# Optimization experiments

Hardware: AMD Instinct MI355X
Metric: run time of the kernel (lower is better)

Reference implementation:

```python
import jax, jax.numpy as jnp
import numpy as np


def setup_inputs() -> dict:
    key = jax.random.key(0)
    k1, k2, k3 = jax.random.split(key, 3)
    B, F, H, W = 16, 16, 256, 256
    inp = jax.random.normal(k1, (B, F, H, W), dtype=jnp.float32)
    target = jax.random.normal(k2, (B, F, H, W), dtype=jnp.float32)
    masks = jax.random.randint(k3, (B, F, H, W), 0, 2).astype(jnp.bool_)
    hull = jnp.zeros((1,), dtype=jnp.int32)  # unused by the module's forward
    return {"input": inp, "target": target, "masks": masks, "hull": hull}


def _masked_mean_per_feature(diff, w):
    # diff: [B,F,H,W]; w: float mask broadcastable to diff. Returns [F] masked means
    # with 0.0 where the mask is empty (matching the torch `if len(diff) > 0` guard).
    s = jnp.sum(diff * w, axis=(0, 2, 3))                               # [F]
    c = jnp.sum(jnp.broadcast_to(w, diff.shape), axis=(0, 2, 3))        # [F]
    return jnp.where(c > 0, s / jnp.maximum(c, 1.0), 0.0)


def reference(input, target, masks, hull):
    diff = jnp.abs(input - target)                                      # [B,F,H,W]
    m = masks.astype(diff.dtype)                                        # feature masks
    m_not = 1.0 - m                                                     # background
    m_all = jnp.any(masks, axis=1, keepdims=True).astype(diff.dtype)    # [B,1,H,W]

    loss_features = jnp.mean(_masked_mean_per_feature(diff, m))
    loss_background = jnp.mean(_masked_mean_per_feature(diff, m_not))
    loss_all_features = jnp.mean(_masked_mean_per_feature(diff, m_all))

    return (loss_features + loss_all_features + loss_background) / 3.0
```

## Files before the change

kernel.cpp:

```cpp
#include <hip/hip_runtime.h>
#include <hip/hip_bf16.h>

constexpr int B = 16, F = 16, H = 256, W = 256;
constexpr int HW = H * W;
constexpr int SPATIAL = B * HW;
constexpr int NBLOCKS = 1024;
constexpr int NTHREADS = 256;
constexpr int NVALS = 65;
constexpr int PLANE4 = HW / 4;
constexpr int BSTRIDE4 = F * PLANE4;

__inline__ __device__ float wave_reduce_sum(float v) {
    #pragma unroll
    for (int o = 32; o > 0; o >>= 1) v += __shfl_down(v, o, 64);
    return v;
}

__global__ __launch_bounds__(NTHREADS) void heatloss_main(
        const float4* __restrict__ inp, const float4* __restrict__ tgt,
        const unsigned int* __restrict__ msk, float* __restrict__ partials) {
    const int g   = blockIdx.x * NTHREADS + threadIdx.x;
    const int b   = g >> 14;
    const int hw4 = g & (PLANE4 - 1);
    const int base = b * BSTRIDE4 + hw4;

    unsigned int m[F];
    #pragma unroll
    for (int f = 0; f < F; f++) m[f] = msk[base + f * PLANE4];

    unsigned int anyu = 0;
    #pragma unroll
    for (int f = 0; f < F; f++) anyu |= m[f];
    const float af0 = (anyu & 0x000000FFu) ? 1.f : 0.f;
    const float af1 = (anyu & 0x0000FF00u) ? 1.f : 0.f;
    const float af2 = (anyu & 0x00FF0000u) ? 1.f : 0.f;
    const float af3 = (anyu & 0xFF000000u) ? 1.f : 0.f;
    const float call = (af0 + af1) + (af2 + af3);

    float s[F], c[F], dtot[F], sall[F];
    #pragma unroll
    for (int f = 0; f < F; f++) {
        const float4 a = inp[base + f * PLANE4];
        const float4 t = tgt[base + f * PLANE4];
        const float d0 = fabsf(a.x - t.x);
        const float d1 = fabsf(a.y - t.y);
        const float d2 = fabsf(a.z - t.z);
        const float d3 = fabsf(a.w - t.w);
        const unsigned int mm = m[f];
        const float m0 = (float)( mm        & 0xFFu);
        const float m1 = (float)((mm >> 8)  & 0xFFu);
        const float m2 = (float)((mm >> 16) & 0xFFu);
        const float m3 = (float)( mm >> 24);
        dtot[f] = (d0 + d1) + (d2 + d3);
        s[f]    = m0 * d0 + m1 * d1 + m2 * d2 + m3 * d3;
        c[f]    = (m0 + m1) + (m2 + m3);
        sall[f] = af0 * d0 + af1 * d1 + af2 * d2 + af3 * d3;
    }

    __shared__ float red[NTHREADS / 64][NVALS];
    const int lane = threadIdx.x & 63;
    const int wave = threadIdx.x >> 6;
    #pragma unroll
    for (int v = 0; v < NVALS; v++) {
        float x = (v < 16) ? s[v]
                : (v < 32) ? c[v - 16]
                : (v < 48) ? dtot[v - 32]
                : (v < 64) ? sall[v - 48]
                : call;
        x = wave_reduce_sum(x);
        if (lane == 0) red[wave][v] = x;
    }
    __syncthreads();
    if (threadIdx.x < NVALS) {
        const int v = threadIdx.x;
        float t = 0.f;
        #pragma unroll
        for (int w2 = 0; w2 < NTHREADS / 64; w2++) t += red[w2][v];
        partials[v * NBLOCKS + blockIdx.x] = t;
    }
}

__global__ __launch_bounds__(512) void heatloss_finalize(
        const float* __restrict__ partials, float* __restrict__ out) {
    __shared__ float vals[NVALS];
    const int wave = threadIdx.x >> 6;
    const int lane = threadIdx.x & 63;
    for (int v = wave; v < NVALS; v += 8) {
        const float* p = partials + v * NBLOCKS;
        float x = 0.f;
        #pragma unroll
        for (int i = 0; i < NBLOCKS / 64; i++) x += p[i * 64 + lane];
        x = wave_reduce_sum(x);
        if (lane == 0) vals[v] = x;
    }
    __syncthreads();
    if (threadIdx.x == 0) {
        const float Nf = (float)SPATIAL;
        const float call = vals[64];
        float lf = 0.f, lbg = 0.f, lall = 0.f;
        #pragma unroll
        for (int f = 0; f < F; f++) {
            const float sf = vals[f], cf = vals[16 + f];
            const float dt = vals[32 + f], sa = vals[48 + f];
            lf += (cf > 0.f) ? sf / cf : 0.f;
            const float sbg = dt - sf, cbg = Nf - cf;
            lbg += (cbg > 0.f) ? sbg / cbg : 0.f;
            lall += (call > 0.f) ? sa / call : 0.f;
        }
        out[0] = (lf / 16.f + lbg / 16.f + lall / 16.f) / 3.f;
    }
}

extern "C" void kernel_launch(void* const* d_in, const int* in_sizes, int n_in,
                              void* d_out, int out_size, void* d_ws, size_t ws_size,
                              hipStream_t stream) {
    const float4*       inp = (const float4*)d_in[0];
    const float4*       tgt = (const float4*)d_in[1];
    const unsigned int* msk = (const unsigned int*)d_in[2];
    float* out      = (float*)d_out;
    float* partials = (float*)d_ws;

    heatloss_main<<<NBLOCKS, NTHREADS, 0, stream>>>(inp, tgt, msk, partials);
    heatloss_finalize<<<1, 512, 0, stream>>>(partials, out);
}
```

Before: 203.6 us.

## Split features across half-waves with 512-thread blocks to raise parallelism

Each wave now covers 32 spatial float4 positions, and each half-wave handles 8 of the 16 features, so every thread does half the loads and keeps half as many accumulators. The any-feature mask is combined across the two halves with a cross-lane shuffle, and the reductions use 32-lane shuffles. Block size doubles to 512 threads with a minimum-occupancy hint, so more memory requests are in flight per CU and register pressure drops. In exchange, the per-block reduction tree grows and coalescing is now in 32-lane (128-byte per float4 row) chunks per half-wave.

```diff
diff --git a/kernel.cpp b/kernel.cpp
--- a/kernel.cpp
+++ b/kernel.cpp
@@ -5,78 +5,88 @@
 constexpr int HW = H * W;
 constexpr int SPATIAL = B * HW;
 constexpr int NBLOCKS = 1024;
-constexpr int NTHREADS = 256;
+constexpr int NTHREADS = 512;
 constexpr int NVALS = 65;
 constexpr int PLANE4 = HW / 4;
 constexpr int BSTRIDE4 = F * PLANE4;
+constexpr int FH = 8;
 
-__inline__ __device__ float wave_reduce_sum(float v) {
+__inline__ __device__ float reduce32(float v) {
     #pragma unroll
-    for (int o = 32; o > 0; o >>= 1) v += __shfl_down(v, o, 64);
+    for (int o = 16; o > 0; o >>= 1) v += __shfl_down(v, o, 32);
     return v;
 }
 
-__global__ __launch_bounds__(NTHREADS) void heatloss_main(
+__global__ __launch_bounds__(NTHREADS, 8) void heatloss_main(
         const float4* __restrict__ inp, const float4* __restrict__ tgt,
         const unsigned int* __restrict__ msk, float* __restrict__ partials) {
-    const int g   = blockIdx.x * NTHREADS + threadIdx.x;
-    const int b   = g >> 14;
-    const int hw4 = g & (PLANE4 - 1);
-    const int base = b * BSTRIDE4 + hw4;
+    const int tid    = threadIdx.x;
+    const int wave   = tid >> 6;
+    const int lane   = tid & 63;
+    const int lane32 = lane & 31;
+    const int half   = lane >> 5;
+    const int g      = (blockIdx.x * 8 + wave) * 32 + lane32;
+    const int b      = g >> 14;
+    const int hw4    = g & (PLANE4 - 1);
+    const int base   = b * BSTRIDE4 + hw4 + half * (FH * PLANE4);
 
-    unsigned int m[F];
+    unsigned int m[FH];
     #pragma unroll
-    for (int f = 0; f < F; f++) m[f] = msk[base + f * PLANE4];
+    for (int j = 0; j < FH; j++) m[j] = msk[base + j * PLANE4];
 
     unsigned int anyu = 0;
     #pragma unroll
-    for (int f = 0; f < F; f++) anyu |= m[f];
+    for (int j = 0; j < FH; j++) anyu |= m[j];
+    anyu |= __shfl_xor(anyu, 32, 64);
     const float af0 = (anyu & 0x000000FFu) ? 1.f : 0.f;
     const float af1 = (anyu & 0x0000FF00u) ? 1.f : 0.f;
     const float af2 = (anyu & 0x00FF0000u) ? 1.f : 0.f;
     const float af3 = (anyu & 0xFF000000u) ? 1.f : 0.f;
-    const float call = (af0 + af1) + (af2 + af3);
+    const float call = (half == 0) ? (af0 + af1) + (af2 + af3) : 0.f;
 
-    float s[F], c[F], dtot[F], sall[F];
+    float s[FH], c[FH], dtot[FH], sall[FH];
     #pragma unroll
-    for (int f = 0; f < F; f++) {
-        const float4 a = inp[base + f * PLANE4];
-        const float4 t = tgt[base + f * PLANE4];
+    for (int j = 0; j < FH; j++) {
+        const float4 a = inp[base + j * PLANE4];
+        const float4 t = tgt[base + j * PLANE4];
         const float d0 = fabsf(a.x - t.x);
         const float d1 = fabsf(a.y - t.y);
         const float d2 = fabsf(a.z - t.z);
         const float d3 = fabsf(a.w - t.w);
-        const unsigned int mm = m[f];
+        const unsigned int mm = m[j];
         const float m0 = (float)( mm        & 0xFFu);
         const float m1 = (float)((mm >> 8)  & 0xFFu);
         const float m2 = (float)((mm >> 16) & 0xFFu);
         const float m3 = (float)( mm >> 24);
-        dtot[f] = (d0 + d1) + (d2 + d3);
-        s[f]    = m0 * d0 + m1 * d1 + m2 * d2 + m3 * d3;
-        c[f]    = (m0 + m1) + (m2 + m3);
-        sall[f] = af0 * d0 + af1 * d1 + af2 * d2 + af3 * d3;
+        dtot[j] = (d0 + d1) + (d2 + d3);
+        s[j]    = m0 * d0 + m1 * d1 + m2 * d2 + m3 * d3;
+        c[j]    = (m0 + m1) + (m2 + m3);
+        sall[j] = af0 * d0 + af1 * d1 + af2 * d2 + af3 * d3;
     }
 
     __shared__ float red[NTHREADS / 64][NVALS];
-    const int lane = threadIdx.x & 63;
-    const int wave = threadIdx.x >> 6;
+    const int fbase = half * FH;
     #pragma unroll
-    for (int v = 0; v < NVALS; v++) {
-        float x = (v < 16) ? s[v]
-                : (v < 32) ? c[v - 16]
-                : (v < 48) ? dtot[v - 32]
-                : (v < 64) ? sall[v - 48]
-                : call;
-        x = wave_reduce_sum(x);
-        if (lane == 0) red[wave][v] = x;
+    for (int j = 0; j < FH; j++) {
+        const float xs = reduce32(s[j]);
+        const float xc = reduce32(c[j]);
+        const float xd = reduce32(dtot[j]);
+        const float xa = reduce32(sall[j]);
+        if (lane32 == 0) {
+            red[wave][ 0 + fbase + j] = xs;
+            red[wave][16 + fbase + j] = xc;
+            red[wave][32 + fbase + j] = xd;
+            red[wave][48 + fbase + j] = xa;
+        }
     }
+    const float xcall = reduce32(call);
+    if (lane == 0) red[wave][64] = xcall;
     __syncthreads();
-    if (threadIdx.x < NVALS) {
-        const int v = threadIdx.x;
+    if (tid < NVALS) {
         float t = 0.f;
         #pragma unroll
-        for (int w2 = 0; w2 < NTHREADS / 64; w2++) t += red[w2][v];
-        partials[v * NBLOCKS + blockIdx.x] = t;
+        for (int w2 = 0; w2 < NTHREADS / 64; w2++) t += red[w2][tid];
+        partials[tid * NBLOCKS + blockIdx.x] = t;
     }
 }
 
@@ -90,7 +100,8 @@
         float x = 0.f;
         #pragma unroll
         for (int i = 0; i < NBLOCKS / 64; i++) x += p[i * 64 + lane];
-        x = wave_reduce_sum(x);
+        #pragma unroll
+        for (int o = 32; o > 0; o >>= 1) x += __shfl_down(x, o, 64);
         if (lane == 0) vals[v] = x;
     }
     __syncthreads();
```

Result: slower. 211.4 us (+3.8%).

## Split loss into any-mask pass and per-feature streaming pass with staged reductions

Applied to the files above, without the earlier changes.

Restructures the single fused kernel into four kernels. The first computes the any-feature mask per pixel into workspace, the second streams input, target and mask per (feature, chunk) block with only four accumulators, and two small kernels then reduce the partials. The aim is to drop the heavy register use of 64 per-thread accumulators and the 65-value shuffle reduction, which should raise occupancy and make the memory stream simpler. In exchange the mask is read twice, a 4 MB any-mask buffer is written and read back, and there are extra kernel launches.

```diff
diff --git a/kernel.cpp b/kernel.cpp
--- a/kernel.cpp
+++ b/kernel.cpp
@@ -4,108 +4,138 @@
 constexpr int B = 16, F = 16, H = 256, W = 256;
 constexpr int HW = H * W;
 constexpr int SPATIAL = B * HW;
-constexpr int NBLOCKS = 1024;
-constexpr int NTHREADS = 256;
 constexpr int NVALS = 65;
-constexpr int PLANE4 = HW / 4;
-constexpr int BSTRIDE4 = F * PLANE4;
+constexpr int PLANE4  = HW / 4;
+constexpr int BSTR4   = F * PLANE4;
+constexpr int POS4    = SPATIAL / 4;
 
-__inline__ __device__ float wave_reduce_sum(float v) {
+constexpr int NB_A = 1024;
+constexpr int NB_B = 2048;
+constexpr int CHUNKS = NB_B / F;
+constexpr int ITER = 8;
+
+constexpr int WS_ANY = 0;
+constexpr int WS_PA  = POS4;
+constexpr int WS_PB  = WS_PA + NB_A;
+constexpr int WS_VAL = WS_PB + 64 * CHUNKS;
+
+
+__global__ __launch_bounds__(256) void heat_any(
+        const unsigned int* __restrict__ msk, unsigned int* __restrict__ any,
+        float* __restrict__ pa) {
+    const int p4 = blockIdx.x * 256 + threadIdx.x;
+    const int b   = p4 >> 14;
+    const int hw4 = p4 & (PLANE4 - 1);
+    const int base = b * BSTR4 + hw4;
+    unsigned int a = 0;
     #pragma unroll
-    for (int o = 32; o > 0; o >>= 1) v += __shfl_down(v, o, 64);
-    return v;
+    for (int f = 0; f < F; f++) a |= msk[base + f * PLANE4];
+    any[p4] = a;
+    float cnt = (float)((a & 1u) + ((a >> 8) & 1u) + ((a >> 16) & 1u) + (a >> 24));
+    #pragma unroll
+    for (int o = 32; o > 0; o >>= 1) cnt += __shfl_down(cnt, o, 64);
+    __shared__ float red[4];
+    if ((threadIdx.x & 63) == 0) red[threadIdx.x >> 6] = cnt;
+    __syncthreads();
+    if (threadIdx.x == 0) pa[blockIdx.x] = (red[0] + red[1]) + (red[2] + red[3]);
 }
 
-__global__ __launch_bounds__(NTHREADS) void heatloss_main(
+__global__ __launch_bounds__(256) void heat_stream(
         const float4* __restrict__ inp, const float4* __restrict__ tgt,
-        const unsigned int* __restrict__ msk, float* __restrict__ partials) {
-    const int g   = blockIdx.x * NTHREADS + threadIdx.x;
-    const int b   = g >> 14;
-    const int hw4 = g & (PLANE4 - 1);
-    const int base = b * BSTRIDE4 + hw4;
+        const unsigned int* __restrict__ msk, const unsigned int* __restrict__ any,
+        float* __restrict__ pb) {
+    const int f     = blockIdx.x & 15;
+    const int chunk = blockIdx.x >> 4;
+    const int t     = threadIdx.x;
+    const int g0    = chunk * (256 * ITER) + t;
 
-    unsigned int m[F];
-    #pragma unroll
-    for (int f = 0; f < F; f++) m[f] = msk[base + f * PLANE4];
-
-    unsigned int anyu = 0;
-    #pragma unroll
-    for (int f = 0; f < F; f++) anyu |= m[f];
-    const float af0 = (anyu & 0x000000FFu) ? 1.f : 0.f;
-    const float af1 = (anyu & 0x0000FF00u) ? 1.f : 0.f;
-    const float af2 = (anyu & 0x00FF0000u) ? 1.f : 0.f;
-    const float af3 = (anyu & 0xFF000000u) ? 1.f : 0.f;
-    const float call = (af0 + af1) + (af2 + af3);
-
-    float s[F], c[F], dtot[F], sall[F];
-    #pragma unroll
-    for (int f = 0; f < F; f++) {
-        const float4 a = inp[base + f * PLANE4];
-        const float4 t = tgt[base + f * PLANE4];
-        const float d0 = fabsf(a.x - t.x);
-        const float d1 = fabsf(a.y - t.y);
-        const float d2 = fabsf(a.z - t.z);
-        const float d3 = fabsf(a.w - t.w);
-        const unsigned int mm = m[f];
+    float s = 0.f, c = 0.f, dt = 0.f, sa = 0.f;
+    #pragma unroll 4
+    for (int i = 0; i < ITER; i++) {
+        const int g   = g0 + i * 256;
+        const int b   = g >> 14;
+        const int hw4 = g & (PLANE4 - 1);
+        const int di  = b * BSTR4 + f * PLANE4 + hw4;
+        const int ai  = b * PLANE4 + hw4;
+        const float4 av = inp[di];
+        const float4 tv = tgt[di];
+        const unsigned int mm = msk[di];
+        const unsigned int aa = any[ai];
+        const float d0 = fabsf(av.x - tv.x);
+        const float d1 = fabsf(av.y - tv.y);
+        const float d2 = fabsf(av.z - tv.z);
+        const float d3 = fabsf(av.w - tv.w);
         const float m0 = (float)( mm        & 0xFFu);
         const float m1 = (float)((mm >> 8)  & 0xFFu);
         const float m2 = (float)((mm >> 16) & 0xFFu);
         const float m3 = (float)( mm >> 24);
-        dtot[f] = (d0 + d1) + (d2 + d3);
-        s[f]    = m0 * d0 + m1 * d1 + m2 * d2 + m3 * d3;
-        c[f]    = (m0 + m1) + (m2 + m3);
-        sall[f] = af0 * d0 + af1 * d1 + af2 * d2 + af3 * d3;
+        const float a0 = (float)( aa        & 0xFFu);
+        const float a1 = (float)((aa >> 8)  & 0xFFu);
+        const float a2 = (float)((aa >> 16) & 0xFFu);
+        const float a3 = (float)( aa >> 24);
+        dt += (d0 + d1) + (d2 + d3);
+        s  += m0 * d0 + m1 * d1 + m2 * d2 + m3 * d3;
+        c  += (m0 + m1) + (m2 + m3);
+        sa += a0 * d0 + a1 * d1 + a2 * d2 + a3 * d3;
     }
 
-    __shared__ float red[NTHREADS / 64][NVALS];
-    const int lane = threadIdx.x & 63;
-    const int wave = threadIdx.x >> 6;
     #pragma unroll
-    for (int v = 0; v < NVALS; v++) {
-        float x = (v < 16) ? s[v]
-                : (v < 32) ? c[v - 16]
-                : (v < 48) ? dtot[v - 32]
-                : (v < 64) ? sall[v - 48]
-                : call;
-        x = wave_reduce_sum(x);
-        if (lane == 0) red[wave][v] = x;
+    for (int o = 32; o > 0; o >>= 1) {
+        s  += __shfl_down(s,  o, 64);
+        c  += __shfl_down(c,  o, 64);
+        dt += __shfl_down(dt, o, 64);
+        sa += __shfl_down(sa, o, 64);
+    }
+    __shared__ float red[4][4];
+    const int wave = t >> 6;
+    if ((t & 63) == 0) {
+        red[wave][0] = s; red[wave][1] = c; red[wave][2] = dt; red[wave][3] = sa;
     }
     __syncthreads();
-    if (threadIdx.x < NVALS) {
-        const int v = threadIdx.x;
-        float t = 0.f;
-        #pragma unroll
-        for (int w2 = 0; w2 < NTHREADS / 64; w2++) t += red[w2][v];
-        partials[v * NBLOCKS + blockIdx.x] = t;
+    if (t < 4) {
+        const float v = red[0][t] + red[1][t] + red[2][t] + red[3][t];
+        pb[(t * 16 + f) * CHUNKS + chunk] = v;
     }
 }
 
-__global__ __launch_bounds__(512) void heatloss_finalize(
-        const float* __restrict__ partials, float* __restrict__ out) {
+__global__ __launch_bounds__(256) void heat_reduce(
+        const float* __restrict__ pa, const float* __restrict__ pb,
+        float* __restrict__ vals) {
+    const int v = blockIdx.x;
+    const int t = threadIdx.x;
+    float x = 0.f;
+    if (v < 64) {
+        if (t < CHUNKS) x = pb[v * CHUNKS + t];
+    } else {
+        #pragma unroll
+        for (int k = 0; k < NB_A / 256; k++) x += pa[t + k * 256];
+    }
+    #pragma unroll
+    for (int o = 32; o > 0; o >>= 1) x += __shfl_down(x, o, 64);
+    __shared__ float red[4];
+    if ((t & 63) == 0) red[t >> 6] = x;
+    __syncthreads();
+    if (t == 0) vals[v] = (red[0] + red[1]) + (red[2] + red[3]);
+}
+
+__global__ __launch_bounds__(128) void heat_combine(
+        const float* __restrict__ vals_in, float* __restrict__ out) {
     __shared__ float vals[NVALS];
-    const int wave = threadIdx.x >> 6;
-    const int lane = threadIdx.x & 63;
-    for (int v = wave; v < NVALS; v += 8) {
-        const float* p = partials + v * NBLOCKS;
-        float x = 0.f;
-        #pragma unroll
-        for (int i = 0; i < NBLOCKS / 64; i++) x += p[i * 64 + lane];
-        x = wave_reduce_sum(x);
-        if (lane == 0) vals[v] = x;
-    }
+    const int t = threadIdx.x;
+    if (t < NVALS) vals[t] = vals_in[t];
     __syncthreads();
-    if (threadIdx.x == 0) {
+    if (t == 0) {
         const float Nf = (float)SPATIAL;
         const float call = vals[64];
         float lf = 0.f, lbg = 0.f, lall = 0.f;
         #pragma unroll
         for (int f = 0; f < F; f++) {
             const float sf = vals[f], cf = vals[16 + f];
-            const float dt = vals[32 + f], sa = vals[48 + f];
+            const float dtv = vals[32 + f], sav = vals[48 + f];
             lf += (cf > 0.f) ? sf / cf : 0.f;
-            const float sbg = dt - sf, cbg = Nf - cf;
+            const float sbg = dtv - sf, cbg = Nf - cf;
             lbg += (cbg > 0.f) ? sbg / cbg : 0.f;
-            lall += (call > 0.f) ? sa / call : 0.f;
+            lall += (call > 0.f) ? sav / call : 0.f;
         }
         out[0] = (lf / 16.f + lbg / 16.f + lall / 16.f) / 3.f;
     }
@@ -117,9 +147,16 @@
     const float4*       inp = (const float4*)d_in[0];
     const float4*       tgt = (const float4*)d_in[1];
     const unsigned int* msk = (const unsigned int*)d_in[2];
-    float* out      = (float*)d_out;
-    float* partials = (float*)d_ws;
+    float* out = (float*)d_out;
+    unsigned int* ws_u = (unsigned int*)d_ws;
+    float*        ws_f = (float*)d_ws;
+    unsigned int* any  = ws_u + WS_ANY;
+    float*        pa   = ws_f + WS_PA;
+    float*        pb   = ws_f + WS_PB;
+    float*        vals = ws_f + WS_VAL;
 
-    heatloss_main<<<NBLOCKS, NTHREADS, 0, stream>>>(inp, tgt, msk, partials);
-    heatloss_finalize<<<1, 512, 0, stream>>>(partials, out);
+    heat_any<<<NB_A, 256, 0, stream>>>(msk, any, pa);
+    heat_stream<<<NB_B, 256, 0, stream>>>(inp, tgt, msk, any, pb);
+    heat_reduce<<<NVALS, 256, 0, stream>>>(pa, pb, vals);
+    heat_combine<<<1, 128, 0, stream>>>(vals, out);
 }
```

After: 185.9 us. -8.7%, faster.
